# Kernel tuning notes

Hardware: AMD Instinct MI355X
Metric: run time of the kernel (lower is better)

Reference implementation:

```python
import jax, jax.numpy as jnp
from jax import lax
import numpy as np


def setup_inputs() -> dict:
    B, P, L, H, T = 4, 160, 128, 768, 9
    rng = np.random.default_rng(0)
    sent_length = rng.integers(L // 2, L + 1, size=B)
    sent_length[0] = L  # ensure max length equals L (pad_packed total_length)
    p2w = np.zeros((B, L, P), dtype=bool)
    for bi in range(B):
        pos = 1  # skip [CLS]
        for w in range(int(sent_length[bi])):
            n = 1 + int(rng.random() < 0.2)  # avg ~1.2 pieces per word
            if pos >= P - 1:
                break
            end = min(pos + n, P - 1)
            p2w[bi, w, pos:end] = True
            pos = end
    masks = np.arange(L)[None, :] < sent_length[:, None]
    labels = rng.integers(0, T, size=(B, L))
    key = jax.random.key(0)
    k1, k2, k3, k4, k5 = jax.random.split(key, 5)
    return {
        "bert_embs": jax.random.normal(k1, (B, P, H), jnp.float32),
        "pieces2word": jnp.asarray(p2w),
        "masks": jnp.asarray(masks),
        "labels": jnp.asarray(labels, jnp.int32),
        "sent_length": jnp.asarray(sent_length, jnp.int32),
        "W": jax.random.normal(k2, (H, T), jnp.float32) * 0.02,
        "b": jnp.zeros((T,), jnp.float32),
        "start_transitions": jax.random.uniform(k3, (T,), jnp.float32, -0.1, 0.1),
        "end_transitions": jax.random.uniform(k4, (T,), jnp.float32, -0.1, 0.1),
        "transitions": jax.random.uniform(k5, (T, T), jnp.float32, -0.1, 0.1),
    }


def crf_log_likelihood(emissions, tags, mask, start_t, end_t, trans):
    # torchcrf CRF forward (batch_first): log p(tags | emissions)
    B, L, T = emissions.shape
    maskf = mask.astype(emissions.dtype)
    barange = jnp.arange(B)
    # numerator: score of the gold tag sequence
    first_tags = tags[:, 0]
    num0 = start_t[first_tags] + emissions[barange, 0, first_tags]

    def num_step(s, inp):
        em_t, tp, tc, m = inp  # em_t: (B,T)
        return s + (trans[tp, tc] + em_t[barange, tc]) * m, None

    num, _ = lax.scan(
        num_step, num0,
        (emissions[:, 1:].transpose(1, 0, 2), tags[:, :-1].T, tags[:, 1:].T, maskf[:, 1:].T),
    )
    last_idx = jnp.sum(mask.astype(jnp.int32), axis=1) - 1
    num = num + end_t[tags[barange, last_idx]]
    # denominator: forward algorithm (log partition)
    alpha0 = start_t[None, :] + emissions[:, 0]  # (B,T)

    def den_step(a, inp):
        em_t, m = inp
        nxt = jax.nn.logsumexp(a[:, :, None] + trans[None, :, :] + em_t[:, None, :], axis=1)
        return jnp.where(m[:, None], nxt, a), None

    alpha, _ = lax.scan(den_step, alpha0, (emissions[:, 1:].transpose(1, 0, 2), mask[:, 1:].T))
    den = jax.nn.logsumexp(alpha + end_t[None, :], axis=1)
    return num - den


def reference(bert_embs, pieces2word, masks, labels, sent_length, W, b,
              start_transitions, end_transitions, transitions):
    min_value = lax.stop_gradient(jnp.min(bert_embs))  # .item() in torch detaches
    # expand + masked_fill + max over pieces: (B, L, P, H) -> (B, L, H)
    expanded = jnp.where(pieces2word[:, :, :, None], bert_embs[:, None, :, :], min_value)
    word_reps = jnp.max(expanded, axis=2)
    # pack_padded/pad_packed zeroes positions beyond sent_length
    word_reps = word_reps * masks[:, :, None].astype(word_reps.dtype)
    logits = word_reps @ W + b  # (B, L, T)
    llh = crf_log_likelihood(logits, labels, masks, start_transitions, end_transitions, transitions)
    loss = -jnp.sum(llh)  # module returns -1 * crf(...) (reduction='sum')
    return (loss, logits)
```

## Files before the change

### kernel.cpp

```cpp
#include <hip/hip_runtime.h>

#define NB 4
#define NP 160
#define NL 128
#define NH 768
#define NT 9
#define NBLK (NB * NL)
#define L2E 1.4426950408889634f
#define LN2 0.6931471805599453f

struct WS {
    float lg[NBLK * NT];
    float part[NBLK];
    int   empty[NBLK];
};

__device__ __forceinline__ float rdlane(float v, int p) {
    return __int_as_float(__builtin_amdgcn_readlane(__float_as_int(v), p));
}

__device__ __forceinline__ float dpp_add(float x) {
    float t;
#define STEP(ctrl, rmask, bc) \
    t = __int_as_float(__builtin_amdgcn_update_dpp(0, __float_as_int(x), ctrl, rmask, 0xf, bc)); \
    x += t;
    STEP(0x111, 0xf, true) STEP(0x112, 0xf, true) STEP(0x114, 0xf, true) STEP(0x118, 0xf, true)
    STEP(0x142, 0xa, false) STEP(0x143, 0xc, false)
#undef STEP
    return x;
}

__device__ __forceinline__ float dpp_fmin(float x) {
    float t;
#define STEP(ctrl, rmask) \
    t = __int_as_float(__builtin_amdgcn_update_dpp(__float_as_int(x), __float_as_int(x), ctrl, rmask, 0xf, false)); \
    x = fminf(x, t);
    STEP(0x111, 0xf) STEP(0x112, 0xf) STEP(0x114, 0xf) STEP(0x118, 0xf)
    STEP(0x142, 0xa) STEP(0x143, 0xc)
#undef STEP
    return x;
}

__device__ __forceinline__ float exp2v(float x) {
    float r; asm("v_exp_f32 %0, %1" : "=v"(r) : "v"(x)); return r;
}
__device__ __forceinline__ float log2v(float x) {
    float r; asm("v_log_f32 %0, %1" : "=v"(r) : "v"(x)); return r;
}

__global__ __launch_bounds__(256) void klogits(
    const float* __restrict__ embs, const void* __restrict__ p2w,
    const void* __restrict__ masks, const float* __restrict__ W,
    const float* __restrict__ bias, float* __restrict__ out_logits, WS* __restrict__ ws)
{
    const int bl = blockIdx.x;
    const int b  = bl / NL;
    const int tid = threadIdx.x;
    const int w = tid >> 6, lane = tid & 63;

    __shared__ int   plist[NP];
    __shared__ int   cnt;
    __shared__ int   isint_sh;
    __shared__ float wmin[4];

    const float4* e4 = (const float4*)(embs + bl * 960);
    float4 mv4 = (tid < 240) ? e4[tid] : make_float4(3.0e38f, 3.0e38f, 3.0e38f, 3.0e38f);
    unsigned char pb = 0;
    if (tid < NP) pb = ((const unsigned char*)p2w)[bl * NP + tid];
    const unsigned char mkb = ((const unsigned char*)masks)[bl];

    if (tid == 0) { isint_sh = (((const unsigned*)masks)[0] <= 1u); cnt = 0; }
    __syncthreads();
    const int is_int = isint_sh;

    int have = 0;
    if (tid < NP) have = is_int ? (((const int*)p2w)[bl * NP + tid] != 0) : (pb != 0);
    if (have) plist[atomicAdd(&cnt, 1)] = tid;

    float m = fminf(fminf(mv4.x, mv4.y), fminf(mv4.z, mv4.w));
    m = dpp_fmin(m);
    if (lane == 63) wmin[w] = m;

    const int mk = is_int ? (((const int*)masks)[bl] != 0) : (mkb != 0);
    __syncthreads();
    if (tid == 0) ws->part[bl] = fminf(fminf(wmin[0], wmin[1]), fminf(wmin[2], wmin[3]));

    const int nc = cnt;
    if (nc == 0) {
        if (tid == 0) ws->empty[bl] = mk ? 1 : 0;
        if (tid < NT) { float v = bias[tid]; out_logits[bl * NT + tid] = v; ws->lg[bl * NT + tid] = v; }
        return;
    }
    if (tid == 0) ws->empty[bl] = 0;

    float wr[12];
    #pragma unroll
    for (int j = 0; j < 12; j++) wr[j] = -3.0e38f;
    for (int i = 0; i < nc; i++) {
        const float* er = embs + (b * NP + plist[i]) * NH;
        #pragma unroll
        for (int j = 0; j < 12; j++) wr[j] = fmaxf(wr[j], er[lane + j * 64]);
    }
    const float mkf = mk ? 1.0f : 0.0f;

    for (int t = w; t < NT; t += 4) {
        float acc = 0.f;
        #pragma unroll
        for (int j = 0; j < 12; j++) acc += wr[j] * W[(lane + j * 64) * NT + t];
        acc = dpp_add(acc);
        if (lane == 63) {
            float v = fmaf(mkf, acc, bias[t]);
            out_logits[bl * NT + t] = v;
            ws->lg[bl * NT + t]     = v;
        }
    }
}

__global__ __launch_bounds__(512) void kcrf(
    const int* __restrict__ labels, const int* __restrict__ sentlen,
    const float* __restrict__ W, const float* __restrict__ bias,
    const float* __restrict__ start_t, const float* __restrict__ end_t,
    const float* __restrict__ trans, WS* __restrict__ ws, float* __restrict__ out)
{
    __shared__ float em_s[NB * NL * NT + 16];
    __shared__ float trs[NT * NT];
    __shared__ int   lab_s[NB * NL];
    __shared__ float llh[NB];
    __shared__ float colsum[NT];
    __shared__ float wmin[8];

    const int tid  = threadIdx.x;
    const int w    = tid >> 6;
    const int lane = tid & 63;

    const float4* s4 = (const float4*)ws->lg;
    float4 lgA = s4[tid];
    float4 lgB = s4[tid + 512];
    float4 lgC = (tid < 128) ? s4[tid + 1024] : make_float4(0, 0, 0, 0);
    int4  labv = (tid < 128) ? ((const int4*)labels)[tid] : make_int4(0, 0, 0, 0);
    float pmv  = ws->part[tid];
    float trv  = (tid < NT * NT) ? trans[tid] : 0.f;

    float4* d4 = (float4*)em_s;
    d4[tid]       = lgA;
    d4[tid + 512] = lgB;
    if (tid < 128) d4[tid + 1024] = lgC;
    if (tid < 128) ((int4*)lab_s)[tid] = labv;
    if (tid < NT * NT) trs[tid] = trv * L2E;

    {
        float mv = dpp_fmin(pmv);
        if (lane == 63) wmin[w] = mv;
    }
    if (w < 4) {
        for (int t = w; t < NT; t += 4) {
            float s = 0.f;
            #pragma unroll
            for (int j = 0; j < 12; j++) s += W[(lane + j * 64) * NT + t];
            s = dpp_add(s);
            if (lane == 63) colsum[t] = s;
        }
    }
    __syncthreads();
    const float minv = fminf(fminf(fminf(wmin[0], wmin[1]), fminf(wmin[2], wmin[3])),
                             fminf(fminf(wmin[4], wmin[5]), fminf(wmin[6], wmin[7])));

    for (int r = tid; r < NBLK; r += 512) {
        if (ws->empty[r]) {
            #pragma unroll
            for (int t = 0; t < NT; t++) {
                float v = fmaf(minv, colsum[t], bias[t]);
                em_s[r * NT + t]    = v;
                out[1 + r * NT + t] = v;
            }
        }
    }
    __syncthreads();

    if (w < 4) {
        const int b   = w;
        const int c   = (lane < NT) ? lane : 0;
        const int len = sentlen[b];
        const float* em  = em_s + b * NL * NT;
        const int*   lab = lab_s + b * NL;

        float nsum = 0.f;
        for (int i = 1 + lane; i < len; i += 64) {
            int tp = lab[i - 1], tc = lab[i];
            nsum = fmaf(em[i * NT + tc], L2E, nsum + trs[tp * NT + tc]);
        }
        nsum = dpp_add(nsum);
        const float nsum_all = rdlane(nsum, 63);

        float tcol[NT];
        #pragma unroll
        for (int p = 0; p < NT; p++) tcol[p] = trs[p * NT + c];
        const float ecol0 = exp2v(tcol[0]);

        float vini = fmaf(em[c], L2E, start_t[c] * L2E);
        float rv0  = rdlane(vini, 0);
        float wrel = vini - rv0;
        float a0abs = rv0;
        float r1 = rdlane(wrel, 1), r2 = rdlane(wrel, 2), r3 = rdlane(wrel, 3);
        float r4 = rdlane(wrel, 4), r5 = rdlane(wrel, 5), r6 = rdlane(wrel, 6);
        float r7 = rdlane(wrel, 7), r8 = rdlane(wrel, 8);

        float em_c = em[NT + c];
        for (int i = 1; i < len; i++) {
            float em_nx = em[(i + 1) * NT + c];
            float e1 = exp2v(r1 + tcol[1]);
            float e2 = exp2v(r2 + tcol[2]);
            float e3 = exp2v(r3 + tcol[3]);
            float e4 = exp2v(r4 + tcol[4]);
            float e5 = exp2v(r5 + tcol[5]);
            float e6 = exp2v(r6 + tcol[6]);
            float e7 = exp2v(r7 + tcol[7]);
            float e8 = exp2v(r8 + tcol[8]);
            float s = (((ecol0 + e1) + (e2 + e3)) + ((e4 + e5) + (e6 + e7))) + e8;
            float v = fmaf(em_c, L2E, log2v(s));
            float nv0 = rdlane(v, 0);
            wrel = v - nv0;
            r1 = rdlane(wrel, 1); r2 = rdlane(wrel, 2); r3 = rdlane(wrel, 3);
            r4 = rdlane(wrel, 4); r5 = rdlane(wrel, 5); r6 = rdlane(wrel, 6);
            r7 = rdlane(wrel, 7); r8 = rdlane(wrel, 8);
            a0abs += nv0;
            em_c = em_nx;
        }

        float xv = wrel + end_t[c] * L2E;
        if (lane == 0) {
            float dv[NT];
            #pragma unroll
            for (int p = 0; p < NT; p++) dv[p] = rdlane(xv, p);
            float mx = fmaxf(fmaxf(fmaxf(dv[0], dv[1]), dv[2]),
                             fmaxf(fmaxf(fmaxf(dv[3], dv[4]), dv[5]),
                                   fmaxf(fmaxf(dv[6], dv[7]), dv[8])));
            float s = 0.f;
            #pragma unroll
            for (int p = 0; p < NT; p++) s += exp2v(dv[p] - mx);
            float den = a0abs + mx + log2v(s);
            int   t0  = lab[0];
            float num = fmaf(em[t0], L2E, nsum_all + start_t[t0] * L2E + end_t[lab[len - 1]] * L2E);
            llh[b] = (num - den) * LN2;
        }
    }
    __syncthreads();
    if (tid == 0) out[0] = -(llh[0] + llh[1] + llh[2] + llh[3]);
}

extern "C" void kernel_launch(void* const* d_in, const int* in_sizes, int n_in,
                              void* d_out, int out_size, void* d_ws, size_t ws_size,
                              hipStream_t stream) {
    const float* embs    = (const float*)d_in[0];
    const void*  p2w     = d_in[1];
    const void*  masks   = d_in[2];
    const int*   labels  = (const int*)d_in[3];
    const int*   sentlen = (const int*)d_in[4];
    const float* W       = (const float*)d_in[5];
    const float* bias    = (const float*)d_in[6];
    const float* start_t = (const float*)d_in[7];
    const float* end_t   = (const float*)d_in[8];
    const float* trans   = (const float*)d_in[9];

    float* out = (float*)d_out;
    WS*    ws  = (WS*)d_ws;

    klogits<<<NBLK, 256, 0, stream>>>(embs, p2w, masks, W, bias, out + 1, ws);
    kcrf<<<1, 512, 0, stream>>>(labels, sentlen, W, bias, start_t, end_t, trans, ws, out);
}
```

Measured before the change: 29.57 us.

## Fuse logits and CRF kernels into one launch with flag-based inter-block sync

Merges the per-word logits kernel and the single-block CRF kernel into one grid, where an extra last block spin-waits on per-row magic flags written with atomic stores before running the CRF reduction. This removes the second kernel launch and the gap between the two kernels. In exchange the CRF block now runs with 256 threads instead of 512. It also depends on the last block being scheduled alongside or after the producers, and it resets the flags at the end for the next call.

After: 30.34 us. +2.6%, slower.

```diff
diff --git a/kernel.cpp b/kernel.cpp
--- a/kernel.cpp
+++ b/kernel.cpp
@@ -8,12 +8,16 @@
 #define NBLK (NB * NL)
 #define L2E 1.4426950408889634f
 #define LN2 0.6931471805599453f
+#define MAGIC 0x5F3D2B19u
 
 struct WS {
-    float lg[NBLK * NT];
-    float part[NBLK];
-    int   empty[NBLK];
+    float    lg[NBLK * NT];
+    float    part[NBLK];
+    unsigned flags[NBLK];
 };
+
+#define AST(p, v) __hip_atomic_store((p), (v), __ATOMIC_RELAXED, __HIP_MEMORY_SCOPE_AGENT)
+#define ALD(p)    __hip_atomic_load((p), __ATOMIC_RELAXED, __HIP_MEMORY_SCOPE_AGENT)
 
 __device__ __forceinline__ float rdlane(float v, int p) {
     return __int_as_float(__builtin_amdgcn_readlane(__float_as_int(v), p));
@@ -48,136 +52,147 @@
     float r; asm("v_log_f32 %0, %1" : "=v"(r) : "v"(x)); return r;
 }
 
-__global__ __launch_bounds__(256) void klogits(
+__global__ __launch_bounds__(256) void kfused(
     const float* __restrict__ embs, const void* __restrict__ p2w,
-    const void* __restrict__ masks, const float* __restrict__ W,
-    const float* __restrict__ bias, float* __restrict__ out_logits, WS* __restrict__ ws)
+    const void* __restrict__ masks, const int* __restrict__ labels,
+    const int* __restrict__ sentlen, const float* __restrict__ W,
+    const float* __restrict__ bias, const float* __restrict__ start_t,
+    const float* __restrict__ end_t, const float* __restrict__ trans,
+    float* __restrict__ out, WS* __restrict__ ws)
 {
-    const int bl = blockIdx.x;
-    const int b  = bl / NL;
+    const int bl  = blockIdx.x;
     const int tid = threadIdx.x;
     const int w = tid >> 6, lane = tid & 63;
 
-    __shared__ int   plist[NP];
-    __shared__ int   cnt;
-    __shared__ int   isint_sh;
-    __shared__ float wmin[4];
-
-    const float4* e4 = (const float4*)(embs + bl * 960);
-    float4 mv4 = (tid < 240) ? e4[tid] : make_float4(3.0e38f, 3.0e38f, 3.0e38f, 3.0e38f);
-    unsigned char pb = 0;
-    if (tid < NP) pb = ((const unsigned char*)p2w)[bl * NP + tid];
-    const unsigned char mkb = ((const unsigned char*)masks)[bl];
-
-    if (tid == 0) { isint_sh = (((const unsigned*)masks)[0] <= 1u); cnt = 0; }
-    __syncthreads();
-    const int is_int = isint_sh;
-
-    int have = 0;
-    if (tid < NP) have = is_int ? (((const int*)p2w)[bl * NP + tid] != 0) : (pb != 0);
-    if (have) plist[atomicAdd(&cnt, 1)] = tid;
-
-    float m = fminf(fminf(mv4.x, mv4.y), fminf(mv4.z, mv4.w));
-    m = dpp_fmin(m);
-    if (lane == 63) wmin[w] = m;
-
-    const int mk = is_int ? (((const int*)masks)[bl] != 0) : (mkb != 0);
-    __syncthreads();
-    if (tid == 0) ws->part[bl] = fminf(fminf(wmin[0], wmin[1]), fminf(wmin[2], wmin[3]));
-
-    const int nc = cnt;
-    if (nc == 0) {
-        if (tid == 0) ws->empty[bl] = mk ? 1 : 0;
-        if (tid < NT) { float v = bias[tid]; out_logits[bl * NT + tid] = v; ws->lg[bl * NT + tid] = v; }
+    if (bl < NBLK) {
+        const int b = bl / NL;
+
+        __shared__ int   plist[NP];
+        __shared__ int   cnt;
+        __shared__ int   isint_sh;
+        __shared__ float wmin[4];
+
+        const float4* e4 = (const float4*)(embs + bl * 960);
+        float4 mv4 = (tid < 240) ? e4[tid] : make_float4(3.0e38f, 3.0e38f, 3.0e38f, 3.0e38f);
+        unsigned char pb = 0;
+        if (tid < NP) pb = ((const unsigned char*)p2w)[bl * NP + tid];
+        const unsigned char mkb = ((const unsigned char*)masks)[bl];
+
+        if (tid == 0) { isint_sh = (((const unsigned*)masks)[0] <= 1u); cnt = 0; }
+        __syncthreads();
+        const int is_int = isint_sh;
+
+        int have = 0;
+        if (tid < NP) have = is_int ? (((const int*)p2w)[bl * NP + tid] != 0) : (pb != 0);
+        if (have) plist[atomicAdd(&cnt, 1)] = tid;
+
+        float m = fminf(fminf(mv4.x, mv4.y), fminf(mv4.z, mv4.w));
+        m = dpp_fmin(m);
+        if (lane == 63) wmin[w] = m;
+
+        const int mk = is_int ? (((const int*)masks)[bl] != 0) : (mkb != 0);
+        __syncthreads();
+        if (tid == 0) {
+            float pm = fminf(fminf(wmin[0], wmin[1]), fminf(wmin[2], wmin[3]));
+            AST(&ws->part[bl], pm);
+        }
+
+        const int nc = cnt;
+        if (nc == 0) {
+            if (tid < NT) {
+                float v = bias[tid];
+                out[1 + bl * NT + tid] = v;
+                AST(&ws->lg[bl * NT + tid], v);
+            }
+        } else {
+            float wr[12];
+            #pragma unroll
+            for (int j = 0; j < 12; j++) wr[j] = -3.0e38f;
+            for (int i = 0; i < nc; i++) {
+                const float* er = embs + (b * NP + plist[i]) * NH;
+                #pragma unroll
+                for (int j = 0; j < 12; j++) wr[j] = fmaxf(wr[j], er[lane + j * 64]);
+            }
+            const float mkf = mk ? 1.0f : 0.0f;
+            for (int t = w; t < NT; t += 4) {
+                float acc = 0.f;
+                #pragma unroll
+                for (int j = 0; j < 12; j++) acc += wr[j] * W[(lane + j * 64) * NT + t];
+                acc = dpp_add(acc);
+                if (lane == 63) {
+                    float v = fmaf(mkf, acc, bias[t]);
+                    out[1 + bl * NT + t] = v;
+                    AST(&ws->lg[bl * NT + t], v);
+                }
+            }
+        }
+
+        asm volatile("s_waitcnt vmcnt(0)" ::: "memory");
+        __syncthreads();
+        if (tid == 0) AST(&ws->flags[bl], MAGIC + ((nc == 0 && mk) ? 1u : 0u));
         return;
     }
-    if (tid == 0) ws->empty[bl] = 0;
-
-    float wr[12];
-    #pragma unroll
-    for (int j = 0; j < 12; j++) wr[j] = -3.0e38f;
-    for (int i = 0; i < nc; i++) {
-        const float* er = embs + (b * NP + plist[i]) * NH;
-        #pragma unroll
-        for (int j = 0; j < 12; j++) wr[j] = fmaxf(wr[j], er[lane + j * 64]);
-    }
-    const float mkf = mk ? 1.0f : 0.0f;
-
-    for (int t = w; t < NT; t += 4) {
-        float acc = 0.f;
-        #pragma unroll
-        for (int j = 0; j < 12; j++) acc += wr[j] * W[(lane + j * 64) * NT + t];
-        acc = dpp_add(acc);
-        if (lane == 63) {
-            float v = fmaf(mkf, acc, bias[t]);
-            out_logits[bl * NT + t] = v;
-            ws->lg[bl * NT + t]     = v;
-        }
-    }
-}
-
-__global__ __launch_bounds__(512) void kcrf(
-    const int* __restrict__ labels, const int* __restrict__ sentlen,
-    const float* __restrict__ W, const float* __restrict__ bias,
-    const float* __restrict__ start_t, const float* __restrict__ end_t,
-    const float* __restrict__ trans, WS* __restrict__ ws, float* __restrict__ out)
-{
+
     __shared__ float em_s[NB * NL * NT + 16];
     __shared__ float trs[NT * NT];
     __shared__ int   lab_s[NB * NL];
     __shared__ float llh[NB];
     __shared__ float colsum[NT];
-    __shared__ float wmin[8];
-
-    const int tid  = threadIdx.x;
-    const int w    = tid >> 6;
-    const int lane = tid & 63;
-
-    const float4* s4 = (const float4*)ws->lg;
-    float4 lgA = s4[tid];
-    float4 lgB = s4[tid + 512];
-    float4 lgC = (tid < 128) ? s4[tid + 1024] : make_float4(0, 0, 0, 0);
-    int4  labv = (tid < 128) ? ((const int4*)labels)[tid] : make_int4(0, 0, 0, 0);
-    float pmv  = ws->part[tid];
-    float trv  = (tid < NT * NT) ? trans[tid] : 0.f;
-
-    float4* d4 = (float4*)em_s;
-    d4[tid]       = lgA;
-    d4[tid + 512] = lgB;
-    if (tid < 128) d4[tid + 1024] = lgC;
-    if (tid < 128) ((int4*)lab_s)[tid] = labv;
-    if (tid < NT * NT) trs[tid] = trv * L2E;
+    __shared__ float wmin2[4];
+
+    if (tid < 128) ((int4*)lab_s)[tid] = ((const int4*)labels)[tid];
+    if (tid < NT * NT) trs[tid] = trans[tid] * L2E;
+    for (int t = w; t < NT; t += 4) {
+        float s = 0.f;
+        #pragma unroll
+        for (int j = 0; j < 12; j++) s += W[(lane + j * 64) * NT + t];
+        s = dpp_add(s);
+        if (lane == 63) colsum[t] = s;
+    }
+
+    unsigned f0, f1;
+    while ((f0 = ALD(&ws->flags[tid])) - MAGIC > 1u) __builtin_amdgcn_s_sleep(1);
+    while ((f1 = ALD(&ws->flags[tid + 256])) - MAGIC > 1u) __builtin_amdgcn_s_sleep(1);
+    __syncthreads();
 
     {
-        float mv = dpp_fmin(pmv);
-        if (lane == 63) wmin[w] = mv;
-    }
-    if (w < 4) {
-        for (int t = w; t < NT; t += 4) {
-            float s = 0.f;
-            #pragma unroll
-            for (int j = 0; j < 12; j++) s += W[(lane + j * 64) * NT + t];
-            s = dpp_add(s);
-            if (lane == 63) colsum[t] = s;
-        }
-    }
-    __syncthreads();
-    const float minv = fminf(fminf(fminf(wmin[0], wmin[1]), fminf(wmin[2], wmin[3])),
-                             fminf(fminf(wmin[4], wmin[5]), fminf(wmin[6], wmin[7])));
-
-    for (int r = tid; r < NBLK; r += 512) {
-        if (ws->empty[r]) {
-            #pragma unroll
-            for (int t = 0; t < NT; t++) {
-                float v = fmaf(minv, colsum[t], bias[t]);
-                em_s[r * NT + t]    = v;
-                out[1 + r * NT + t] = v;
-            }
-        }
-    }
-    __syncthreads();
-
-    if (w < 4) {
+        float mv = fminf(ALD(&ws->part[tid]), ALD(&ws->part[tid + 256]));
+        mv = dpp_fmin(mv);
+        if (lane == 63) wmin2[w] = mv;
+    }
+    {
+        const unsigned long long* lg8 = (const unsigned long long*)ws->lg;
+        #pragma unroll
+        for (int r = 0; r < 9; r++) {
+            int i = tid + r * 256;
+            unsigned long long v = ALD(&lg8[i]);
+            em_s[2 * i]     = __int_as_float((unsigned)v);
+            em_s[2 * i + 1] = __int_as_float((unsigned)(v >> 32));
+        }
+    }
+    __syncthreads();
+    const float minv = fminf(fminf(wmin2[0], wmin2[1]), fminf(wmin2[2], wmin2[3]));
+
+    if (f0 == MAGIC + 1u) {
+        #pragma unroll
+        for (int t = 0; t < NT; t++) {
+            float v = fmaf(minv, colsum[t], bias[t]);
+            em_s[tid * NT + t]    = v;
+            out[1 + tid * NT + t] = v;
+        }
+    }
+    if (f1 == MAGIC + 1u) {
+        const int r = tid + 256;
+        #pragma unroll
+        for (int t = 0; t < NT; t++) {
+            float v = fmaf(minv, colsum[t], bias[t]);
+            em_s[r * NT + t]    = v;
+            out[1 + r * NT + t] = v;
+        }
+    }
+    __syncthreads();
+
+    {
         const int b   = w;
         const int c   = (lane < NT) ? lane : 0;
         const int len = sentlen[b];
@@ -246,6 +261,9 @@
     }
     __syncthreads();
     if (tid == 0) out[0] = -(llh[0] + llh[1] + llh[2] + llh[3]);
+
+    AST(&ws->flags[tid], 0u);
+    AST(&ws->flags[tid + 256], 0u);
 }
 
 extern "C" void kernel_launch(void* const* d_in, const int* in_sizes, int n_in,
@@ -265,6 +283,6 @@
     float* out = (float*)d_out;
     WS*    ws  = (WS*)d_ws;
 
-    klogits<<<NBLK, 256, 0, stream>>>(embs, p2w, masks, W, bias, out + 1, ws);
-    kcrf<<<1, 512, 0, stream>>>(labels, sentlen, W, bias, start_t, end_t, trans, ws, out);
-}
+    kfused<<<NBLK + 1, 256, 0, stream>>>(embs, p2w, masks, labels, sentlen, W, bias,
+                                         start_t, end_t, trans, out, ws);
+}
```
